# Performance work log

Hardware: AMD Instinct MI355X
Metric: run time of the kernel (lower is better)

The kernel has to match this reference:

```python
import jax, jax.numpy as jnp
import numpy as np

N_NODES = 50000
N_EDGES = 640000
HIDDEN = 128
EDGE_DIM = 3


def _glorot(key, shape):
    fan_in, fan_out = shape[0], shape[1]
    lim = (6.0 / (fan_in + fan_out)) ** 0.5
    return jax.random.uniform(key, shape, jnp.float32, -lim, lim)


def setup_inputs() -> dict:
    key = jax.random.key(0)
    ks = jax.random.split(key, 12)
    x = jax.random.normal(ks[0], (N_NODES, HIDDEN), jnp.float32)
    edge_index = jax.random.randint(ks[1], (2, N_EDGES), 0, N_NODES, jnp.int64)
    edge_attr = jax.random.normal(ks[2], (N_EDGES, EDGE_DIM), jnp.float32)
    params = {
        "W_msg1": _glorot(ks[3], (2 * HIDDEN + EDGE_DIM, HIDDEN)),
        "b_msg1": jnp.zeros((HIDDEN,), jnp.float32),
        "W_msg2": _glorot(ks[4], (HIDDEN, HIDDEN)),
        "b_msg2": jnp.zeros((HIDDEN,), jnp.float32),
        "W_gate": _glorot(ks[5], (2 * HIDDEN, HIDDEN)),
        "b_gate": jnp.zeros((HIDDEN,), jnp.float32),
        "W_upd1": _glorot(ks[6], (2 * HIDDEN, HIDDEN)),
        "b_upd1": jnp.zeros((HIDDEN,), jnp.float32),
        "W_upd2": _glorot(ks[7], (HIDDEN, HIDDEN)),
        "b_upd2": jnp.zeros((HIDDEN,), jnp.float32),
        "ln_gamma": jnp.ones((HIDDEN,), jnp.float32),
        "ln_beta": jnp.zeros((HIDDEN,), jnp.float32),
    }
    return dict(x=x, edge_index=edge_index, edge_attr=edge_attr, **params)


def reference(x, edge_index, edge_attr, W_msg1, b_msg1, W_msg2, b_msg2,
              W_gate, b_gate, W_upd1, b_upd1, W_upd2, b_upd2, ln_gamma, ln_beta):
    src, dst = edge_index[0], edge_index[1]
    source = x[src]            # [E, H]
    target = x[dst]            # [E, H]
    msg_in = jnp.concatenate([source, target, edge_attr], axis=-1)  # [E, 2H+edge_dim]
    h = jax.nn.relu(msg_in @ W_msg1 + b_msg1)  # dropout is identity in eval
    messages = h @ W_msg2 + b_msg2             # [E, H]
    aggregated = jax.ops.segment_sum(messages, dst, num_segments=x.shape[0])  # [N, H]
    upd_in = jnp.concatenate([x, aggregated], axis=-1)  # [N, 2H]
    gate = jax.nn.sigmoid(upd_in @ W_gate + b_gate)
    update = jax.nn.relu(upd_in @ W_upd1 + b_upd1) @ W_upd2 + b_upd2
    out = gate * update + (1.0 - gate) * x
    # LayerNorm (eps=1e-5, matching torch default)
    mu = jnp.mean(out, axis=-1, keepdims=True)
    var = jnp.var(out, axis=-1, keepdims=True)
    normed = (out - mu) * jax.lax.rsqrt(var + 1e-5)
    return normed * ln_gamma + ln_beta
```

## Files before the change

kernel.cpp:

```cpp
#include <hip/hip_runtime.h>
#include <hip/hip_bf16.h>

#define HID 128

typedef __attribute__((ext_vector_type(8))) short short8;
typedef __attribute__((ext_vector_type(4))) float f32x4;

__device__ __forceinline__ unsigned short f2bf(float f) {
    unsigned int u = __builtin_bit_cast(unsigned int, f);
    u += 0x7FFFu + ((u >> 16) & 1u);
    return (unsigned short)(u >> 16);
}
__device__ __forceinline__ float bf2f(unsigned short h) {
    unsigned int u = ((unsigned int)h) << 16;
    return __builtin_bit_cast(float, u);
}

__global__ void prep_all(const float* __restrict__ Wm1,
                         const float* __restrict__ Wg,  const float* __restrict__ Wu1,
                         const float* __restrict__ Wm2, const float* __restrict__ bm2,
                         const float* __restrict__ Wu2,
                         unsigned short* __restrict__ W1f,
                         unsigned short* __restrict__ WgH,  float* __restrict__ bcg,
                         unsigned short* __restrict__ Wu1H, float* __restrict__ bcu,
                         unsigned short* __restrict__ Wu2H,
                         unsigned* __restrict__ cnt, int N)
{
    int b = blockIdx.x;
    if (b < 16) {
        int t = b * 256 + threadIdx.x;
        if (t < 4096) {
            int lane = t & 63, nt = (t >> 6) & 7, ks = t >> 9;
            int kb  = ks * 32 + ((lane >> 4) << 3);
            int col = (nt << 4) + (lane & 15);
            union { unsigned short u[8]; uint4 q; } p;
            #pragma unroll
            for (int j = 0; j < 8; ++j) p.u[j] = f2bf(Wm1[(size_t)(kb + j) * 128 + col]);
            *(uint4*)(W1f + (size_t)t * 8) = p.q;
        }
    } else if (b < 272) {
        const bool isG = (b < 144);
        const float* Wtop = isG ? Wg : Wu1;
        unsigned short* Wh = isG ? WgH : Wu1H;
        float* bc = isG ? bcg : bcu;
        int lb = b - (isG ? 16 : 144);
        int t = lb * 256 + threadIdx.x;
        if (t < 32768) {
            int j = t & 7, lane = (t >> 3) & 63, nt = (t >> 9) & 7, ks = t >> 12;
            int r   = ks * 32 + ((lane >> 4) << 3) + j;
            int col = (nt << 4) + (lane & 15);
            float w;
            if (r < 128) {
                w = Wtop[(size_t)r * 128 + col];
            } else {
                const float* a = Wm2 + (size_t)(r - 128) * 128;
                float s = 0.f;
                for (int k = 0; k < 128; ++k)
                    s = fmaf(a[k], Wtop[(size_t)(128 + k) * 128 + col], s);
                w = s;
            }
            Wh[t] = f2bf(w);
        }
        if (lb == 0 && threadIdx.x < 128) {
            int jj = threadIdx.x;
            float s = 0.f;
            for (int k = 0; k < 128; ++k)
                s = fmaf(bm2[k], Wtop[(size_t)(128 + k) * 128 + jj], s);
            bc[jj] = s;
        }
    } else if (b < 280) {
        int t = (b - 272) * 256 + threadIdx.x;
        if (t < 2048) {
            int lane = t & 63, nt = (t >> 6) & 7, ks = t >> 9;
            int kb  = ks * 32 + ((lane >> 4) << 3);
            int col = (nt << 4) + (lane & 15);
            union { unsigned short u[8]; uint4 q; } p;
            #pragma unroll
            for (int j = 0; j < 8; ++j) p.u[j] = f2bf(Wu2[(size_t)(kb + j) * 128 + col]);
            *(uint4*)(Wu2H + (size_t)t * 8) = p.q;
        }
    } else {
        int t = (b - 280) * 256 + threadIdx.x;
        int i = t * 4;
        if (i + 3 < N) {
            *(uint4*)(cnt + i) = make_uint4(0u, 0u, 0u, 0u);
        } else {
            for (int k = 0; k < 4 && i + k < N; ++k) cnt[i + k] = 0u;
        }
    }
}

__global__ void hist_k(const int* __restrict__ ei, unsigned* __restrict__ cnt, int E) {
    int e = blockIdx.x * 256 + threadIdx.x;
    if (e < E) atomicAdd(&cnt[ei[E + e]], 1u);
}

__global__ void scan_k(const unsigned* __restrict__ cnt, unsigned* __restrict__ cur, int n) {
    __shared__ unsigned wsum[16];
    int tid = threadIdx.x, lane = tid & 63, w = tid >> 6;
    unsigned carry = 0;
    for (int base = 0; base < n; base += 4096) {
        int i = base + tid * 4;
        unsigned v0 = 0, v1 = 0, v2 = 0, v3 = 0;
        if (i + 3 < n) {
            uint4 q = *(const uint4*)(cnt + i);
            v0 = q.x; v1 = q.y; v2 = q.z; v3 = q.w;
        } else {
            if (i < n)     v0 = cnt[i];
            if (i + 1 < n) v1 = cnt[i + 1];
            if (i + 2 < n) v2 = cnt[i + 2];
            if (i + 3 < n) v3 = cnt[i + 3];
        }
        unsigned t0 = v0, t1 = t0 + v1, t2 = t1 + v2, t3 = t2 + v3;
        unsigned s = t3;
        #pragma unroll
        for (int off = 1; off < 64; off <<= 1) {
            unsigned t = __shfl_up(s, off);
            if (lane >= off) s += t;
        }
        if (lane == 63) wsum[w] = s;
        __syncthreads();
        if (tid < 16) {
            unsigned t = wsum[tid];
            #pragma unroll
            for (int off = 1; off < 16; off <<= 1) {
                unsigned u = __shfl_up(t, off);
                if (tid >= off) t += u;
            }
            wsum[tid] = t;
        }
        __syncthreads();
        unsigned woff = (w == 0) ? 0u : wsum[w - 1];
        unsigned excl = carry + woff + (s - t3);
        if (i < n)     cur[i]     = excl;
        if (i + 1 < n) cur[i + 1] = excl + t0;
        if (i + 2 < n) cur[i + 2] = excl + t1;
        if (i + 3 < n) cur[i + 3] = excl + t2;
        unsigned tot = wsum[15];
        __syncthreads();
        carry += tot;
    }
}

__global__ void scatter_k(const int* __restrict__ ei, const float* __restrict__ ea,
                          unsigned* __restrict__ cur, uint4* __restrict__ rec, int E) {
    int e = blockIdx.x * 256 + threadIdx.x;
    if (e >= E) return;
    int d = ei[E + e];
    unsigned pos = atomicAdd(&cur[d], 1u);
    uint4 r;
    r.x = (unsigned)ei[e];
    r.y = __builtin_bit_cast(unsigned, ea[(size_t)e * 3 + 0]);
    r.z = __builtin_bit_cast(unsigned, ea[(size_t)e * 3 + 1]);
    r.w = __builtin_bit_cast(unsigned, ea[(size_t)e * 3 + 2]);
    rec[pos] = r;
}

__global__ __launch_bounds__(256, 2)
void s1t_gemm(const float* __restrict__ x, const unsigned short* __restrict__ W1f,
              unsigned short* __restrict__ S1b, unsigned short* __restrict__ Tb, int N)
{
    __shared__ alignas(16) unsigned short sW[32768];
    const int tid  = threadIdx.x;
    for (int i = tid; i < 4096; i += 256)
        ((uint4*)sW)[i] = ((const uint4*)W1f)[i];
    __syncthreads();

    const int lane = tid & 63;
    const int wid  = tid >> 6;
    const int n0   = (blockIdx.x * 4 + wid) * 16;
    if (n0 >= N) return;
    const int arow = lane & 15;
    const int g4   = lane >> 4;

    int nr = n0 + arow; if (nr >= N) nr = N - 1;
    const float* px = x + (size_t)nr * 128 + g4 * 8;

    short8 af[4];
    #pragma unroll
    for (int ks = 0; ks < 4; ++ks) {
        float4 v0 = *(const float4*)(px + ks * 32);
        float4 v1 = *(const float4*)(px + ks * 32 + 4);
        float v[8] = { v0.x, v0.y, v0.z, v0.w, v1.x, v1.y, v1.z, v1.w };
        #pragma unroll
        for (int j = 0; j < 8; ++j) af[ks][j] = (short)f2bf(v[j]);
    }

    f32x4 s1[8], tt[8];
    #pragma unroll
    for (int i = 0; i < 8; ++i) { s1[i] = (f32x4)0.f; tt[i] = (f32x4)0.f; }
    #pragma unroll
    for (int ks = 0; ks < 4; ++ks) {
        #pragma unroll
        for (int nt = 0; nt < 8; ++nt) {
            short8 b1 = *(const short8*)(sW + (size_t)((ks * 8 + nt) * 64 + lane) * 8);
            short8 b2 = *(const short8*)(sW + (size_t)(((ks + 4) * 8 + nt) * 64 + lane) * 8);
            s1[nt] = __builtin_amdgcn_mfma_f32_16x16x32_bf16(af[ks], b1, s1[nt], 0, 0, 0);
            tt[nt] = __builtin_amdgcn_mfma_f32_16x16x32_bf16(af[ks], b2, tt[nt], 0, 0, 0);
        }
    }
    #pragma unroll
    for (int nt = 0; nt < 8; ++nt) {
        int col = nt * 16 + arow;
        #pragma unroll
        for (int r = 0; r < 4; ++r) {
            int node = n0 + g4 * 4 + r;
            if (node < N) {
                S1b[(size_t)node * 128 + col] = f2bf(s1[nt][r]);
                Tb [(size_t)node * 128 + col] = f2bf(tt[nt][r]);
            }
        }
    }
}

__global__ __launch_bounds__(256, 8)
void csr_edge_k(const unsigned short* __restrict__ S1b, const unsigned short* __restrict__ Tb,
                const uint4* __restrict__ rec,
                const unsigned* __restrict__ cnt, const unsigned* __restrict__ cur,
                const float* __restrict__ W1tail, const float* __restrict__ bm1,
                float* __restrict__ HS, int N)
{
    const int lane = threadIdx.x & 63;
    const int wid  = threadIdx.x >> 6;
    const int gw   = blockIdx.x * 4 + wid;
    const int stride = gridDim.x * 4;
    const int c2 = lane * 2;

    const float w00 = W1tail[c2],       w01 = W1tail[c2 + 1];
    const float w10 = W1tail[128 + c2], w11 = W1tail[128 + c2 + 1];
    const float w20 = W1tail[256 + c2], w21 = W1tail[256 + c2 + 1];
    const float b0  = bm1[c2],          b1v = bm1[c2 + 1];

    for (int d = gw; d < N; d += stride) {
        int e1 = (int)cur[d];
        int c  = (int)cnt[d];
        int e0 = e1 - c;
        unsigned tv = *(const unsigned*)(Tb + (size_t)d * 128 + c2);
        float t0 = bf2f((unsigned short)(tv & 0xffff)) + b0;
        float t1 = bf2f((unsigned short)(tv >> 16))    + b1v;
        float a0 = 0.f, a1 = 0.f;
        if (c > 0) {
            uint4 r0 = rec[e0];
            uint4 r1 = (e0 + 1 < e1) ? rec[e0 + 1] : r0;
            uint4 r2 = (e0 + 2 < e1) ? rec[e0 + 2] : r0;
            uint4 r3 = (e0 + 3 < e1) ? rec[e0 + 3] : r0;
            unsigned s0 = *(const unsigned*)(S1b + (size_t)r0.x * 128 + c2);
            unsigned s1 = (e0 + 1 < e1)
                ? *(const unsigned*)(S1b + (size_t)r1.x * 128 + c2) : 0u;
            for (int e = e0; e < e1; ++e) {
                float x0 = __builtin_bit_cast(float, r0.y);
                float x1 = __builtin_bit_cast(float, r0.z);
                float x2 = __builtin_bit_cast(float, r0.w);
                float h0 = bf2f((unsigned short)(s0 & 0xffff)) + t0;
                float h1 = bf2f((unsigned short)(s0 >> 16))    + t1;
                h0 = fmaf(x0, w00, h0); h0 = fmaf(x1, w10, h0); h0 = fmaf(x2, w20, h0);
                h1 = fmaf(x0, w01, h1); h1 = fmaf(x1, w11, h1); h1 = fmaf(x2, w21, h1);
                a0 += fmaxf(h0, 0.f);
                a1 += fmaxf(h1, 0.f);
                r0 = r1; r1 = r2; r2 = r3;
                if (e + 4 < e1) r3 = rec[e + 4];
                s0 = s1;
                if (e + 2 < e1) s1 = *(const unsigned*)(S1b + (size_t)r1.x * 128 + c2);
            }
        }
        float2 o; o.x = a0; o.y = a1;
        *(float2*)(HS + (size_t)d * 128 + c2) = o;
    }
}

__global__ __launch_bounds__(256, 8)
void atomic_edge_k(const unsigned short* __restrict__ S1b, const unsigned short* __restrict__ Tb,
                   const int* __restrict__ ei, const float* __restrict__ ea,
                   const float* __restrict__ W1tail, const float* __restrict__ bm1,
                   float* __restrict__ HS, int E)
{
    const int lane = threadIdx.x & 63;
    const int wid  = threadIdx.x >> 6;
    const int gw   = blockIdx.x * 4 + wid;
    const int stride = gridDim.x * 4;
    const int c2 = lane * 2;

    const float w00 = W1tail[c2],       w01 = W1tail[c2 + 1];
    const float w10 = W1tail[128 + c2], w11 = W1tail[128 + c2 + 1];
    const float w20 = W1tail[256 + c2], w21 = W1tail[256 + c2 + 1];
    const float b0  = bm1[c2],          b1v = bm1[c2 + 1];

    for (int e = gw; e < E; e += stride) {
        int s = ei[e], d = ei[E + e];
        float x0 = ea[(size_t)e * 3 + 0];
        float x1 = ea[(size_t)e * 3 + 1];
        float x2 = ea[(size_t)e * 3 + 2];
        unsigned tv = *(const unsigned*)(Tb + (size_t)d * 128 + c2);
        unsigned sv = *(const unsigned*)(S1b + (size_t)s * 128 + c2);
        float h0 = bf2f((unsigned short)(sv & 0xffff)) + bf2f((unsigned short)(tv & 0xffff)) + b0;
        float h1 = bf2f((unsigned short)(sv >> 16))    + bf2f((unsigned short)(tv >> 16))    + b1v;
        h0 = fmaf(x0, w00, h0); h0 = fmaf(x1, w10, h0); h0 = fmaf(x2, w20, h0);
        h1 = fmaf(x0, w01, h1); h1 = fmaf(x1, w11, h1); h1 = fmaf(x2, w21, h1);
        unsafeAtomicAdd(HS + (size_t)d * 128 + c2,     fmaxf(h0, 0.f));
        unsafeAtomicAdd(HS + (size_t)d * 128 + c2 + 1, fmaxf(h1, 0.f));
    }
}

__global__ __launch_bounds__(256, 2)
void node_mfma(const float* __restrict__ x,
               const float* __restrict__ HS,
               const unsigned* __restrict__ cnt,
               const float* __restrict__ bcg, const float* __restrict__ bcu,
               const unsigned short* __restrict__ WgH,
               const unsigned short* __restrict__ Wu1H,
               const unsigned short* __restrict__ Wu2H,
               const float* __restrict__ bg, const float* __restrict__ bu1,
               const float* __restrict__ bu2,
               const float* __restrict__ gamma, const float* __restrict__ beta,
               float* __restrict__ out, int N)
{
    __shared__ alignas(16) char smem[65536];

    const int tid  = threadIdx.x;
    const int lane = tid & 63;
    const int wid  = tid >> 6;
    const int n0   = (blockIdx.x * 4 + wid) * 16;

    const int arow = lane & 15;
    const int g4   = lane >> 4;

    int nr = n0 + arow; if (nr >= N) nr = N - 1;
    if (nr < 0) nr = 0;
    const float* px = x  + (size_t)nr * 128 + g4 * 8;
    const float* pa = HS + (size_t)nr * 128 + g4 * 8;

    short8 ah[8], al[8];
    #pragma unroll
    for (int ks = 0; ks < 8; ++ks) {
        const float* p = (ks < 4) ? (px + ks * 32) : (pa + (ks - 4) * 32);
        float4 v0 = *(const float4*)p;
        float4 v1 = *(const float4*)(p + 4);
        float v[8] = { v0.x, v0.y, v0.z, v0.w, v1.x, v1.y, v1.z, v1.w };
        #pragma unroll
        for (int j = 0; j < 8; ++j) {
            unsigned short h = f2bf(v[j]);
            ah[ks][j] = (short)h;
            al[ks][j] = (short)f2bf(v[j] - bf2f(h));
        }
    }

    float degf[4];
    #pragma unroll
    for (int r = 0; r < 4; ++r) {
        int node = n0 + g4 * 4 + r;
        degf[r] = (node >= 0 && node < N) ? (float)cnt[node] : 0.f;
    }

    uint4* buf0 = (uint4*)smem;
    uint4* buf1 = (uint4*)(smem + 16384);

    {
        int idx = tid, idx2 = tid + 256;
        buf0[idx]        = ((const uint4*)WgH )[idx];
        buf0[idx2]       = ((const uint4*)WgH )[idx2];
        buf0[512 + idx]  = ((const uint4*)Wu1H)[idx];
        buf0[512 + idx2] = ((const uint4*)Wu1H)[idx2];
    }
    __syncthreads();

    f32x4 ga[8], ua[8];
    #pragma unroll
    for (int i = 0; i < 8; ++i) { ga[i] = (f32x4)0.f; ua[i] = (f32x4)0.f; }

    for (int ks = 0; ks < 8; ++ks) {
        const unsigned short* sB = (const unsigned short*)((ks & 1) ? buf1 : buf0);
        uint4 tg0, tg1, tu0, tu1;
        if (ks < 7) {
            int idx = tid, idx2 = tid + 256;
            tg0 = ((const uint4*)WgH )[(ks + 1) * 512 + idx];
            tg1 = ((const uint4*)WgH )[(ks + 1) * 512 + idx2];
            tu0 = ((const uint4*)Wu1H)[(ks + 1) * 512 + idx];
            tu1 = ((const uint4*)Wu1H)[(ks + 1) * 512 + idx2];
        }
        #pragma unroll
        for (int nt = 0; nt < 8; ++nt) {
            size_t o = (size_t)(nt * 64 + lane) * 8;
            short8 bh = *(const short8*)(sB + o);
            short8 uh = *(const short8*)(sB + 4096 + o);
            ga[nt] = __builtin_amdgcn_mfma_f32_16x16x32_bf16(ah[ks], bh, ga[nt], 0, 0, 0);
            ga[nt] = __builtin_amdgcn_mfma_f32_16x16x32_bf16(al[ks], bh, ga[nt], 0, 0, 0);
            ua[nt] = __builtin_amdgcn_mfma_f32_16x16x32_bf16(ah[ks], uh, ua[nt], 0, 0, 0);
            ua[nt] = __builtin_amdgcn_mfma_f32_16x16x32_bf16(al[ks], uh, ua[nt], 0, 0, 0);
        }
        if (ks < 7) {
            uint4* nb = (ks & 1) ? buf0 : buf1;
            int idx = tid, idx2 = tid + 256;
            nb[idx]        = tg0;
            nb[idx2]       = tg1;
            nb[512 + idx]  = tu0;
            nb[512 + idx2] = tu1;
        }
        __syncthreads();
    }

    #pragma unroll
    for (int nt = 0; nt < 8; ++nt) {
        int col = nt * 16 + arow;
        float bgc = bcg[col], buc = bcu[col];
        #pragma unroll
        for (int r = 0; r < 4; ++r) {
            ga[nt][r] = fmaf(degf[r], bgc, ga[nt][r]);
            ua[nt][r] = fmaf(degf[r], buc, ua[nt][r]);
        }
    }

    char* Hw = smem + 32768 + wid * 8192;
    #pragma unroll
    for (int nt = 0; nt < 8; ++nt) {
        int col = nt * 16 + arow;
        float b1 = bu1[col];
        #pragma unroll
        for (int r = 0; r < 4; ++r) {
            int row = g4 * 4 + r;
            float u = fmaxf(ua[nt][r] + b1, 0.f);
            unsigned short h = f2bf(u);
            unsigned short l = f2bf(u - bf2f(h));
            unsigned int pk = (unsigned int)h | ((unsigned int)l << 16);
            *(unsigned int*)(Hw + row * 512 + ((col * 4) ^ ((row & 15) << 4))) = pk;
        }
    }

    #pragma unroll
    for (int nt = 0; nt < 8; ++nt) {
        int col = nt * 16 + arow;
        float b = bg[col];
        #pragma unroll
        for (int r = 0; r < 4; ++r)
            ga[nt][r] = 1.f / (1.f + expf(-(ga[nt][r] + b)));
    }

    {
        int idx = tid, idx2 = tid + 256;
        buf0[idx]  = ((const uint4*)Wu2H)[idx];
        buf0[idx2] = ((const uint4*)Wu2H)[idx2];
    }
    __syncthreads();

    f32x4 u2[8];
    #pragma unroll
    for (int i = 0; i < 8; ++i) u2[i] = (f32x4)0.f;
    for (int ks = 0; ks < 4; ++ks) {
        const unsigned short* sB = (const unsigned short*)((ks & 1) ? buf1 : buf0);
        uint4 t0v, t1v;
        if (ks < 3) {
            int idx = tid, idx2 = tid + 256;
            t0v = ((const uint4*)Wu2H)[(ks + 1) * 512 + idx];
            t1v = ((const uint4*)Wu2H)[(ks + 1) * 512 + idx2];
        }
        int b0 = ks * 128 + g4 * 32;
        unsigned int q0[4], q1[4];
        *(uint4*)q0 = *(const uint4*)(Hw + arow * 512 + ( b0       ^ (arow << 4)));
        *(uint4*)q1 = *(const uint4*)(Hw + arow * 512 + ((b0 + 16) ^ (arow << 4)));
        short8 a2h, a2l;
        #pragma unroll
        for (int j = 0; j < 4; ++j) {
            a2h[j]     = (short)(q0[j] & 0xffff);
            a2l[j]     = (short)(q0[j] >> 16);
            a2h[4 + j] = (short)(q1[j] & 0xffff);
            a2l[4 + j] = (short)(q1[j] >> 16);
        }
        #pragma unroll
        for (int nt = 0; nt < 8; ++nt) {
            size_t o = (size_t)(nt * 64 + lane) * 8;
            short8 bh = *(const short8*)(sB + o);
            u2[nt] = __builtin_amdgcn_mfma_f32_16x16x32_bf16(a2h, bh, u2[nt], 0, 0, 0);
            u2[nt] = __builtin_amdgcn_mfma_f32_16x16x32_bf16(a2l, bh, u2[nt], 0, 0, 0);
        }
        if (ks < 3) {
            uint4* nb = (ks & 1) ? buf0 : buf1;
            int idx = tid, idx2 = tid + 256;
            nb[idx]  = t0v;
            nb[idx2] = t1v;
        }
        __syncthreads();
    }

    float s[4]  = {0.f, 0.f, 0.f, 0.f};
    float ss[4] = {0.f, 0.f, 0.f, 0.f};
    #pragma unroll
    for (int nt = 0; nt < 8; ++nt) {
        int col = nt * 16 + arow;
        float b2 = bu2[col];
        #pragma unroll
        for (int r = 0; r < 4; ++r) {
            int node = n0 + g4 * 4 + r;
            int nc = (node >= 0 && node < N) ? node : 0;
            float xv = x[(size_t)nc * 128 + col];
            float g  = ga[nt][r];
            float o  = g * (u2[nt][r] + b2) + (1.f - g) * xv;
            u2[nt][r] = o;
            s[r]  += o;
            ss[r] += o * o;
        }
    }
    #pragma unroll
    for (int off = 8; off >= 1; off >>= 1) {
        #pragma unroll
        for (int r = 0; r < 4; ++r) {
            s[r]  += __shfl_xor(s[r],  off);
            ss[r] += __shfl_xor(ss[r], off);
        }
    }
    float mu[4], rstd[4];
    #pragma unroll
    for (int r = 0; r < 4; ++r) {
        mu[r] = s[r] * (1.f / 128.f);
        float var = ss[r] * (1.f / 128.f) - mu[r] * mu[r];
        rstd[r] = rsqrtf(var + 1e-5f);
    }
    #pragma unroll
    for (int nt = 0; nt < 8; ++nt) {
        int col = nt * 16 + arow;
        float gm = gamma[col], bt = beta[col];
        #pragma unroll
        for (int r = 0; r < 4; ++r) {
            int node = n0 + g4 * 4 + r;
            if (node >= 0 && node < N)
                out[(size_t)node * 128 + col] = (u2[nt][r] - mu[r]) * rstd[r] * gm + bt;
        }
    }
}

extern "C" void kernel_launch(void* const* d_in, const int* in_sizes, int n_in,
                              void* d_out, int out_size, void* d_ws, size_t ws_size,
                              hipStream_t stream)
{
    const float* x    = (const float*)d_in[0];
    const int*   ei   = (const int*)  d_in[1];
    const float* ea   = (const float*)d_in[2];
    const float* Wm1  = (const float*)d_in[3];
    const float* bm1  = (const float*)d_in[4];
    const float* Wm2  = (const float*)d_in[5];
    const float* bm2  = (const float*)d_in[6];
    const float* Wg   = (const float*)d_in[7];
    const float* bg   = (const float*)d_in[8];
    const float* Wu1  = (const float*)d_in[9];
    const float* bu1  = (const float*)d_in[10];
    const float* Wu2  = (const float*)d_in[11];
    const float* bu2  = (const float*)d_in[12];
    const float* gmma = (const float*)d_in[13];
    const float* beta = (const float*)d_in[14];
    float* out = (float*)d_out;

    const int N = in_sizes[0] / HID;
    const int E = in_sizes[1] / 2;

    unsigned short* S1b  = (unsigned short*)d_ws;
    unsigned short* Tb   = S1b + (size_t)N * HID;
    float*          HS   = (float*)(Tb + (size_t)N * HID);
    unsigned short* W1f  = (unsigned short*)(HS + (size_t)N * HID);
    unsigned short* WgH  = W1f + 32768;
    unsigned short* Wu1H = WgH + 32768;
    unsigned short* Wu2H = Wu1H + 32768;
    float*          bcg  = (float*)(Wu2H + 16384);
    float*          bcu  = bcg + 128;
    unsigned*       cnt  = (unsigned*)(bcu + 128);
    unsigned*       cur  = cnt + N;
    uint4*          rec  = (uint4*)(cur + N);
    rec = (uint4*)(((size_t)rec + 15) & ~(size_t)15);
    size_t need_sort = (size_t)((char*)(rec + E) - (char*)d_ws);
    const bool tierA = (ws_size >= need_sort);

    int zblocks = ((N + 3) / 4 + 255) / 256;
    prep_all<<<dim3(280 + zblocks), dim3(256), 0, stream>>>(
        Wm1, Wg, Wu1, Wm2, bm2, Wu2, W1f, WgH, bcg, Wu1H, bcu, Wu2H, cnt, N);

    s1t_gemm<<<dim3((N + 63) / 64), dim3(256), 0, stream>>>(x, W1f, S1b, Tb, N);

    hist_k<<<dim3((E + 255) / 256), dim3(256), 0, stream>>>(ei, cnt, E);

    if (tierA) {
        scan_k<<<dim3(1), dim3(1024), 0, stream>>>(cnt, cur, N);
        scatter_k<<<dim3((E + 255) / 256), dim3(256), 0, stream>>>(ei, ea, cur, rec, E);
        csr_edge_k<<<dim3(2048), dim3(256), 0, stream>>>(
            S1b, Tb, rec, cnt, cur, Wm1 + 256 * HID, bm1, HS, N);
    } else {
        hipMemsetAsync(HS, 0, (size_t)N * HID * sizeof(float), stream);
        atomic_edge_k<<<dim3(2048), dim3(256), 0, stream>>>(
            S1b, Tb, ei, ea, Wm1 + 256 * HID, bm1, HS, E);
    }

    node_mfma<<<dim3((N + 63) / 64), dim3(256), 0, stream>>>(
        x, HS, cnt, bcg, bcu,
        WgH, Wu1H, Wu2H,
        bg, bu1, bu2, gmma, beta, out, N);
}
```

Baseline: 228.6 us.

## Fuse destination histogram into S1/T GEMM kernel and unroll CSR edge loop

The separate histogram kernel is removed. Its atomic counting of destination degrees now runs as a grid-stride loop at the start of the S1/T GEMM kernel, which saves one launch and lets the atomics overlap with the GEMM. The CSR edge aggregation loop is also rewritten from a rotating software-prefetch pipeline into a 4-way unrolled body. That body issues four record loads and four gathered S1 loads before computing, followed by a scalar remainder loop. The unroll adds more independent loads in flight but gives up prefetching across iterations and may raise register pressure.

```diff
diff --git a/kernel.cpp b/kernel.cpp
--- a/kernel.cpp
+++ b/kernel.cpp
@@ -90,11 +90,6 @@
     }
 }
 
-__global__ void hist_k(const int* __restrict__ ei, unsigned* __restrict__ cnt, int E) {
-    int e = blockIdx.x * 256 + threadIdx.x;
-    if (e < E) atomicAdd(&cnt[ei[E + e]], 1u);
-}
-
 __global__ void scan_k(const unsigned* __restrict__ cnt, unsigned* __restrict__ cur, int n) {
     __shared__ unsigned wsum[16];
     int tid = threadIdx.x, lane = tid & 63, w = tid >> 6;
@@ -157,11 +152,16 @@
 }
 
 __global__ __launch_bounds__(256, 2)
-void s1t_gemm(const float* __restrict__ x, const unsigned short* __restrict__ W1f,
-              unsigned short* __restrict__ S1b, unsigned short* __restrict__ Tb, int N)
+void s1t_hist_k(const float* __restrict__ x, const unsigned short* __restrict__ W1f,
+                unsigned short* __restrict__ S1b, unsigned short* __restrict__ Tb, int N,
+                const int* __restrict__ ei, unsigned* __restrict__ cnt, int E)
 {
     __shared__ alignas(16) unsigned short sW[32768];
     const int tid  = threadIdx.x;
+
+    for (int e = blockIdx.x * 256 + tid; e < E; e += gridDim.x * 256)
+        atomicAdd(&cnt[ei[E + e]], 1u);
+
     for (int i = tid; i < 4096; i += 256)
         ((uint4*)sW)[i] = ((const uint4*)W1f)[i];
     __syncthreads();
@@ -239,30 +239,71 @@
         float t0 = bf2f((unsigned short)(tv & 0xffff)) + b0;
         float t1 = bf2f((unsigned short)(tv >> 16))    + b1v;
         float a0 = 0.f, a1 = 0.f;
-        if (c > 0) {
-            uint4 r0 = rec[e0];
-            uint4 r1 = (e0 + 1 < e1) ? rec[e0 + 1] : r0;
-            uint4 r2 = (e0 + 2 < e1) ? rec[e0 + 2] : r0;
-            uint4 r3 = (e0 + 3 < e1) ? rec[e0 + 3] : r0;
-            unsigned s0 = *(const unsigned*)(S1b + (size_t)r0.x * 128 + c2);
-            unsigned s1 = (e0 + 1 < e1)
-                ? *(const unsigned*)(S1b + (size_t)r1.x * 128 + c2) : 0u;
-            for (int e = e0; e < e1; ++e) {
-                float x0 = __builtin_bit_cast(float, r0.y);
-                float x1 = __builtin_bit_cast(float, r0.z);
-                float x2 = __builtin_bit_cast(float, r0.w);
-                float h0 = bf2f((unsigned short)(s0 & 0xffff)) + t0;
-                float h1 = bf2f((unsigned short)(s0 >> 16))    + t1;
+
+        int e = e0;
+        for (; e + 4 <= e1; e += 4) {
+            uint4 ra = rec[e];
+            uint4 rb = rec[e + 1];
+            uint4 rc = rec[e + 2];
+            uint4 rd = rec[e + 3];
+            unsigned sa = *(const unsigned*)(S1b + (size_t)ra.x * 128 + c2);
+            unsigned sb = *(const unsigned*)(S1b + (size_t)rb.x * 128 + c2);
+            unsigned sc = *(const unsigned*)(S1b + (size_t)rc.x * 128 + c2);
+            unsigned sd = *(const unsigned*)(S1b + (size_t)rd.x * 128 + c2);
+            {
+                float h0 = bf2f((unsigned short)(sa & 0xffff)) + t0;
+                float h1 = bf2f((unsigned short)(sa >> 16))    + t1;
+                float x0 = __builtin_bit_cast(float, ra.y);
+                float x1 = __builtin_bit_cast(float, ra.z);
+                float x2 = __builtin_bit_cast(float, ra.w);
                 h0 = fmaf(x0, w00, h0); h0 = fmaf(x1, w10, h0); h0 = fmaf(x2, w20, h0);
                 h1 = fmaf(x0, w01, h1); h1 = fmaf(x1, w11, h1); h1 = fmaf(x2, w21, h1);
-                a0 += fmaxf(h0, 0.f);
-                a1 += fmaxf(h1, 0.f);
-                r0 = r1; r1 = r2; r2 = r3;
-                if (e + 4 < e1) r3 = rec[e + 4];
-                s0 = s1;
-                if (e + 2 < e1) s1 = *(const unsigned*)(S1b + (size_t)r1.x * 128 + c2);
+                a0 += fmaxf(h0, 0.f); a1 += fmaxf(h1, 0.f);
             }
-        }
+            {
+                float h0 = bf2f((unsigned short)(sb & 0xffff)) + t0;
+                float h1 = bf2f((unsigned short)(sb >> 16))    + t1;
+                float x0 = __builtin_bit_cast(float, rb.y);
+                float x1 = __builtin_bit_cast(float, rb.z);
+                float x2 = __builtin_bit_cast(float, rb.w);
+                h0 = fmaf(x0, w00, h0); h0 = fmaf(x1, w10, h0); h0 = fmaf(x2, w20, h0);
+                h1 = fmaf(x0, w01, h1); h1 = fmaf(x1, w11, h1); h1 = fmaf(x2, w21, h1);
+                a0 += fmaxf(h0, 0.f); a1 += fmaxf(h1, 0.f);
+            }
+            {
+                float h0 = bf2f((unsigned short)(sc & 0xffff)) + t0;
+                float h1 = bf2f((unsigned short)(sc >> 16))    + t1;
+                float x0 = __builtin_bit_cast(float, rc.y);
+                float x1 = __builtin_bit_cast(float, rc.z);
+                float x2 = __builtin_bit_cast(float, rc.w);
+                h0 = fmaf(x0, w00, h0); h0 = fmaf(x1, w10, h0); h0 = fmaf(x2, w20, h0);
+                h1 = fmaf(x0, w01, h1); h1 = fmaf(x1, w11, h1); h1 = fmaf(x2, w21, h1);
+                a0 += fmaxf(h0, 0.f); a1 += fmaxf(h1, 0.f);
+            }
+            {
+                float h0 = bf2f((unsigned short)(sd & 0xffff)) + t0;
+                float h1 = bf2f((unsigned short)(sd >> 16))    + t1;
+                float x0 = __builtin_bit_cast(float, rd.y);
+                float x1 = __builtin_bit_cast(float, rd.z);
+                float x2 = __builtin_bit_cast(float, rd.w);
+                h0 = fmaf(x0, w00, h0); h0 = fmaf(x1, w10, h0); h0 = fmaf(x2, w20, h0);
+                h1 = fmaf(x0, w01, h1); h1 = fmaf(x1, w11, h1); h1 = fmaf(x2, w21, h1);
+                a0 += fmaxf(h0, 0.f); a1 += fmaxf(h1, 0.f);
+            }
+        }
+        for (; e < e1; ++e) {
+            uint4 r = rec[e];
+            unsigned sv = *(const unsigned*)(S1b + (size_t)r.x * 128 + c2);
+            float h0 = bf2f((unsigned short)(sv & 0xffff)) + t0;
+            float h1 = bf2f((unsigned short)(sv >> 16))    + t1;
+            float x0 = __builtin_bit_cast(float, r.y);
+            float x1 = __builtin_bit_cast(float, r.z);
+            float x2 = __builtin_bit_cast(float, r.w);
+            h0 = fmaf(x0, w00, h0); h0 = fmaf(x1, w10, h0); h0 = fmaf(x2, w20, h0);
+            h1 = fmaf(x0, w01, h1); h1 = fmaf(x1, w11, h1); h1 = fmaf(x2, w21, h1);
+            a0 += fmaxf(h0, 0.f); a1 += fmaxf(h1, 0.f);
+        }
+
         float2 o; o.x = a0; o.y = a1;
         *(float2*)(HS + (size_t)d * 128 + c2) = o;
     }
@@ -570,9 +611,8 @@
     prep_all<<<dim3(280 + zblocks), dim3(256), 0, stream>>>(
         Wm1, Wg, Wu1, Wm2, bm2, Wu2, W1f, WgH, bcg, Wu1H, bcu, Wu2H, cnt, N);
 
-    s1t_gemm<<<dim3((N + 63) / 64), dim3(256), 0, stream>>>(x, W1f, S1b, Tb, N);
-
-    hist_k<<<dim3((E + 255) / 256), dim3(256), 0, stream>>>(ei, cnt, E);
+    s1t_hist_k<<<dim3((N + 63) / 64), dim3(256), 0, stream>>>(
+        x, W1f, S1b, Tb, N, ei, cnt, E);
 
     if (tierA) {
         scan_k<<<dim3(1), dim3(1024), 0, stream>>>(cnt, cur, N);
```

Measured after the change: 199.6 us. -12.7%, faster.
